# Optimization experiments

Hardware: AMD Instinct MI355X
Metric: run time of the kernel (lower is better)

Reference implementation:

```python
import jax, jax.numpy as jnp
import numpy as np

NUM_HEADS = 8


def setup_inputs() -> dict:
    key = jax.random.key(0)
    k1, k2, k3 = jax.random.split(key, 3)
    B, C, D, H, W = 2, 512, 32, 32, 32
    x = jax.random.normal(k1, (B, C, D, H, W), dtype=jnp.float32)
    w_qkv = jax.random.normal(k2, (3 * C, C), dtype=jnp.float32) * 0.02
    b_qkv = jnp.zeros((3 * C,), dtype=jnp.float32)
    w_out = jax.random.normal(k3, (C, C), dtype=jnp.float32) * 0.02
    b_out = jnp.zeros((C,), dtype=jnp.float32)
    return {"x": x, "w_qkv": w_qkv, "b_qkv": b_qkv, "w_out": w_out, "b_out": b_out}


def reference(x, w_qkv, b_qkv, w_out, b_out):
    B, C, D, H, W = x.shape
    nh = NUM_HEADS
    hd = C // nh
    # 1x1x1 conv3d == pointwise linear over channel dim
    qkv = jnp.einsum('bcdhw,oc->bodhw', x, w_qkv) + b_qkv[None, :, None, None, None]
    q, k, v = jnp.split(qkv, 3, axis=1)  # each [B,C,D,H,W]

    def to_heads(t):
        # [B,C,D,H,W] -> [B,nh,hd,D,H,W] -> [B,H,W,nh,D,hd]
        return t.reshape(B, nh, hd, D, H, W).transpose(0, 4, 5, 1, 3, 2)

    q, k, v = to_heads(q), to_heads(k), to_heads(v)
    scale = hd ** -0.5
    # attention along the depth axis D: attn [B,H,W,nh,D,D]
    attn = jnp.einsum('bhwnic,bhwnjc->bhwnij', q, k) * scale
    attn = jax.nn.softmax(attn, axis=-1)
    out = jnp.einsum('bhwnij,bhwnjc->bhwnic', attn, v)  # [B,H,W,nh,D,hd]
    # [B,H,W,nh,D,hd] -> [B,nh,hd,D,H,W] -> [B,C,D,H,W]
    out = out.transpose(0, 3, 5, 4, 1, 2).reshape(B, C, D, H, W)
    out = jnp.einsum('bcdhw,oc->bodhw', out, w_out) + b_out[None, :, None, None, None]
    return out + x
```

## Files before the change

### kernel.cpp

```cpp
#include <hip/hip_runtime.h>


typedef __bf16 bf16x8 __attribute__((ext_vector_type(8)));
typedef float  f32x4  __attribute__((ext_vector_type(4)));
typedef float  f32x16 __attribute__((ext_vector_type(16)));

__device__ __forceinline__ float b2f(unsigned int u) {
    union { float f; unsigned int i; } x; x.i = u << 16; return x.f;
}
__device__ __forceinline__ unsigned short f2b(float f) {
    union { float f; unsigned int i; } x; x.f = f;
    unsigned int r = x.i + 0x7FFFu + ((x.i >> 16) & 1u);
    return (unsigned short)(r >> 16);
}
__device__ __forceinline__ unsigned int cvtpk(float lo, float hi) {
    unsigned int r;
    asm("v_cvt_pk_bf16_f32 %0, %1, %2" : "=v"(r) : "v"(lo), "v"(hi));
    return r;
}
__device__ __forceinline__ f32x4 mfma16(bf16x8 a, bf16x8 b, f32x4 c) {
    return __builtin_amdgcn_mfma_f32_16x16x32_bf16(a, b, c, 0, 0, 0);
}
__device__ __forceinline__ f32x16 mfma32(bf16x8 a, bf16x8 b, f32x16 c) {
    return __builtin_amdgcn_mfma_f32_32x32x16_bf16(a, b, c, 0, 0, 0);
}
__device__ __forceinline__ void gload16(const void* g, void* l) {
    __builtin_amdgcn_global_load_lds((const unsigned int*)g, (unsigned int*)l, 16, 0, 0);
}

__global__ __launch_bounds__(256) void xprep3(const float* __restrict__ x,
                                              const float* __restrict__ wq_f,
                                              const float* __restrict__ wo_f,
                                              unsigned short* __restrict__ xB,
                                              unsigned short* __restrict__ wT,
                                              unsigned short* __restrict__ wo_bf) {
    const int bid = blockIdx.x;
    const int tid = threadIdx.x;
    if (bid < 2048) {
        __shared__ __align__(16) char tile[32768];
        const int ck = bid & 7, dq = (bid >> 3) & 3, h = (bid >> 5) & 31, b = bid >> 10;

        const int cg = tid & 31;
        const int dl = tid >> 5;
        const int d  = dq * 8 + dl;
        const float* p0 = x + (size_t)b * 16777216 + (size_t)(ck * 64 + cg * 2) * 32768 + d * 1024 + h * 32;
        const float* p1 = p0 + 32768;
        const int cb = (cg * 4) ^ (dl << 4);
        #pragma unroll
        for (int k = 0; k < 8; ++k) {
            float4 a0 = *(const float4*)(p0 + 4 * k);
            float4 a1 = *(const float4*)(p1 + 4 * k);
            *(unsigned int*)(tile + dl * 4096 + (4 * k + 0) * 128 + cb) = cvtpk(a0.x, a1.x);
            *(unsigned int*)(tile + dl * 4096 + (4 * k + 1) * 128 + cb) = cvtpk(a0.y, a1.y);
            *(unsigned int*)(tile + dl * 4096 + (4 * k + 2) * 128 + cb) = cvtpk(a0.z, a1.z);
            *(unsigned int*)(tile + dl * 4096 + (4 * k + 3) * 128 + cb) = cvtpk(a0.w, a1.w);
        }
        __syncthreads();
        const int odl = tid & 7, ot = (tid >> 3) & 7, okb = tid >> 6;
        #pragma unroll
        for (int i = 0; i < 8; ++i) {
            const int wg = i >> 1, kkl = i & 1;
            const int cbyte = (kkl * 64 + okb * 16) ^ (odl << 4);
            uint4 v = *(const uint4*)(tile + odl * 4096 + (wg * 8 + ot) * 128 + cbyte);
            const int G  = (b * 32 + h) * 4 + wg;
            const int kk = ck * 2 + kkl;
            *(uint4*)(xB + (size_t)G * 131072 + kk * 8192 + okb * 2048 +
                      (ot * 32 + dq * 8 + odl) * 8) = v;
        }
    } else {
        const int gidx = (bid - 2048) * 256 + tid;
        if (gidx < 98304) {
            const int r  = gidx % 192;
            const int qd = gidx / 192;
            const int kb = qd & 3, kk = (qd >> 2) & 15, n = qd >> 6;
            const int R  = (r >> 6) * 512 + n * 64 + (r & 63);
            const float* s = wq_f + R * 512 + kk * 32 + kb * 8;
            float4 a0 = *(const float4*)s;
            float4 a1 = *(const float4*)(s + 4);
            *(uint4*)(wT + (size_t)gidx * 8) =
                make_uint4(cvtpk(a0.x, a0.y), cvtpk(a0.z, a0.w), cvtpk(a1.x, a1.y), cvtpk(a1.z, a1.w));
        } else {
            const int g2 = gidx - 98304;
            const float* s = wo_f + (size_t)g2 * 8;
            float4 a0 = *(const float4*)s;
            float4 a1 = *(const float4*)(s + 4);
            *(uint4*)(wo_bf + (size_t)g2 * 8) =
                make_uint4(cvtpk(a0.x, a0.y), cvtpk(a0.z, a0.w), cvtpk(a1.x, a1.y), cvtpk(a1.z, a1.w));
        }
    }
}

__global__ __launch_bounds__(256, 2)
void axial_ab4(const unsigned short* __restrict__ xB,
               const unsigned short* __restrict__ wT,
               const float* __restrict__ bq,
               unsigned short* __restrict__ ao)
{
    __shared__ __align__(16) char lds[74496];
    const int SA0 = 0, SB0 = 24576;
    const int QT0 = 0, KT0 = 16384, VT0 = 32768, P0 = 49152, BIAS0 = 73728;
    float* bias_s = (float*)(lds + BIAS0);

    const int bid = blockIdx.x;
    const int vid = (bid & 7) * 256 + (bid >> 3);
    const int n   = vid & 7;
    const int G   = vid >> 3;
    const int b   = G >> 7, h = (G >> 2) & 31, wg = G & 3;
    const int sbase = b * 32768 + h * 32 + wg * 8;

    const int tid = threadIdx.x;
    const int wv  = tid >> 6;
    const int l   = tid & 63;
    const int l31 = l & 31;
    const int hh  = l >> 5;
    const int wm  = wv >> 1;
    const int wn  = wv & 1;

    const unsigned short* wA = wT + (size_t)n * 98304;
    const unsigned short* xG = xB + (size_t)G * 131072;

    auto stageA = [&](int kk, int sl) {
        #pragma unroll
        for (int i = 0; i < 3; ++i) {
            const int j = wv * 3 + i;
            gload16(wA + kk * 6144 + j * 512 + l * 8, lds + SA0 + sl * 12288 + j * 1024);
        }
    };
    auto stageB = [&](int kk, int sl) {
        #pragma unroll
        for (int i = 0; i < 4; ++i) {
            const int j = wv * 4 + i;
            gload16(xG + kk * 8192 + j * 512 + l * 8, lds + SB0 + sl * 16384 + j * 1024);
        }
    };

    f32x16 acc[3][4];
    #pragma unroll
    for (int mf = 0; mf < 3; ++mf)
        #pragma unroll
        for (int nf = 0; nf < 4; ++nf) acc[mf][nf] = (f32x16)0.f;

    auto gphase = [&](int sa, int sb) {
        #pragma unroll
        for (int ks = 0; ks < 2; ++ks) {
            const int kb = ks * 2 + hh;
            bf16x8 af[3], bfr[4];
            #pragma unroll
            for (int mf = 0; mf < 3; ++mf)
                af[mf] = *(const bf16x8*)(lds + SA0 + sa * 12288 + kb * 3072 +
                                          (wm * 96 + mf * 32 + l31) * 16);
            #pragma unroll
            for (int nf = 0; nf < 4; ++nf)
                bfr[nf] = *(const bf16x8*)(lds + SB0 + sb * 16384 + kb * 4096 +
                                           (wn * 128 + nf * 32 + l31) * 16);
            #pragma unroll
            for (int mf = 0; mf < 3; ++mf)
                #pragma unroll
                for (int nf = 0; nf < 4; ++nf)
                    acc[mf][nf] = mfma32(af[mf], bfr[nf], acc[mf][nf]);
        }
    };

    stageA(0, 0); stageB(0, 0); stageB(1, 1);
    asm volatile("s_waitcnt vmcnt(4)" ::: "memory");
    __builtin_amdgcn_s_barrier();
    __builtin_amdgcn_sched_barrier(0);

    #pragma unroll
    for (int kk = 0; kk < 16; ++kk) {
        if (kk < 15) stageA(kk + 1, (kk + 1) & 1);
        if (kk < 14) stageB(kk + 2, (kk + 2) % 3);
        __builtin_amdgcn_s_setprio(1);
        gphase(kk & 1, kk % 3);
        __builtin_amdgcn_s_setprio(0);
        asm volatile("s_waitcnt lgkmcnt(0)" ::: "memory");
        if (kk < 14)       { asm volatile("s_waitcnt vmcnt(4)" ::: "memory"); }
        else if (kk == 14) { asm volatile("s_waitcnt vmcnt(0)" ::: "memory"); }
        __builtin_amdgcn_s_barrier();
        __builtin_amdgcn_sched_barrier(0);
    }

    if (tid < 192) bias_s[tid] = bq[(tid >> 6) * 512 + n * 64 + (tid & 63)];
    __syncthreads();

    #pragma unroll
    for (int ph = 0; ph < 2; ++ph) {
        if (wn == ph) {
            #pragma unroll
            for (int mf = 0; mf < 3; ++mf) {
                const int m0 = wm * 96 + mf * 32;
                #pragma unroll
                for (int nf = 0; nf < 4; ++nf) {
                    const int tl = nf;
                    const int d  = l31;
                    const f32x16 v = acc[mf][nf];
                    if (m0 < 128) {
                        const int base = (m0 < 64) ? QT0 : KT0;
                        const int c0g  = (m0 & 63) >> 3;
                        #pragma unroll
                        for (int p = 0; p < 4; ++p) {
                            float4 bb = *(const float4*)(bias_s + m0 + 8 * p + 4 * hh);
                            unsigned int u0 = cvtpk(v[4 * p]     + bb.x, v[4 * p + 1] + bb.y);
                            unsigned int u1 = cvtpk(v[4 * p + 2] + bb.z, v[4 * p + 3] + bb.w);
                            *(uint2*)(lds + base + tl * 4096 + d * 128 +
                                      (((c0g + p) ^ (d & 7)) << 4) + 8 * hh) = make_uint2(u0, u1);
                        }
                    } else {
                        const int e0 = m0 - 128;
                        const int jj = tl * 32 + l31;
                        #pragma unroll
                        for (int reg = 0; reg < 16; ++reg) {
                            const int e = e0 + (reg & 3) + 8 * (reg >> 2) + 4 * hh;
                            *(unsigned short*)(lds + VT0 + e * 256 +
                                               (((jj >> 3) ^ (e & 7)) << 4) + ((2 * jj) & 15)) =
                                f2b(v[reg]);
                        }
                    }
                }
            }
        }
        __syncthreads();

        {
            const int t  = wv;
            const int qg = l >> 4;
            f32x4 sacc[2][2];
            sacc[0][0] = (f32x4)0.f; sacc[0][1] = (f32x4)0.f;
            sacc[1][0] = (f32x4)0.f; sacc[1][1] = (f32x4)0.f;
            #pragma unroll
            for (int kh = 0; kh < 2; ++kh) {
                bf16x8 qa[2], kb_[2];
                #pragma unroll
                for (int mt = 0; mt < 2; ++mt) {
                    const int i = mt * 16 + (l & 15);
                    qa[mt] = *(const bf16x8*)(lds + QT0 + t * 4096 + i * 128 +
                                              (((kh * 4 + qg) ^ (i & 7)) << 4));
                }
                #pragma unroll
                for (int nt = 0; nt < 2; ++nt) {
                    const int jj = nt * 16 + (l & 15);
                    kb_[nt] = *(const bf16x8*)(lds + KT0 + t * 4096 + jj * 128 +
                                               (((kh * 4 + qg) ^ (jj & 7)) << 4));
                }
                #pragma unroll
                for (int mt = 0; mt < 2; ++mt)
                    #pragma unroll
                    for (int nt = 0; nt < 2; ++nt)
                        sacc[mt][nt] = mfma16(qa[mt], kb_[nt], sacc[mt][nt]);
            }
            #pragma unroll
            for (int mt = 0; mt < 2; ++mt) {
                #pragma unroll
                for (int reg = 0; reg < 4; ++reg) {
                    float s0 = sacc[mt][0][reg] * 0.125f;
                    float s1 = sacc[mt][1][reg] * 0.125f;
                    float m = fmaxf(s0, s1);
                    m = fmaxf(m, __shfl_xor(m, 1));
                    m = fmaxf(m, __shfl_xor(m, 2));
                    m = fmaxf(m, __shfl_xor(m, 4));
                    m = fmaxf(m, __shfl_xor(m, 8));
                    float p0 = __expf(s0 - m);
                    float p1 = __expf(s1 - m);
                    float ss = p0 + p1;
                    ss += __shfl_xor(ss, 1);
                    ss += __shfl_xor(ss, 2);
                    ss += __shfl_xor(ss, 4);
                    ss += __shfl_xor(ss, 8);
                    float inv = 1.0f / ss;
                    const int i = mt * 16 + 4 * qg + reg;
                    #pragma unroll
                    for (int nt = 0; nt < 2; ++nt) {
                        const int j = nt * 16 + (l & 15);
                        *(unsigned short*)(lds + P0 + t * 2048 + i * 64 +
                                           (((j >> 3) ^ (i & 3)) << 4) + ((2 * j) & 15)) =
                            f2b((nt ? p1 : p0) * inv);
                    }
                }
            }
            asm volatile("s_waitcnt lgkmcnt(0)" ::: "memory");
            __builtin_amdgcn_sched_barrier(0);

            f32x16 oa[2];
            oa[0] = (f32x16)0.f; oa[1] = (f32x16)0.f;
            #pragma unroll
            for (int ks = 0; ks < 2; ++ks) {
                bf16x8 pb = *(const bf16x8*)(lds + P0 + t * 2048 + l31 * 64 +
                                             (((ks * 2 + hh) ^ (l31 & 3)) << 4));
                #pragma unroll
                for (int cf = 0; cf < 2; ++cf) {
                    const int c = cf * 32 + l31;
                    bf16x8 vv = *(const bf16x8*)(lds + VT0 + c * 256 +
                                                 (((t * 4 + ks * 2 + hh) ^ (c & 7)) << 4));
                    oa[cf] = mfma32(vv, pb, oa[cf]);
                }
            }
            const size_t srow = (size_t)(sbase + l31 * 1024 + ph * 4 + t) * 512 + n * 64;
            #pragma unroll
            for (int cf = 0; cf < 2; ++cf) {
                #pragma unroll
                for (int p = 0; p < 4; ++p) {
                    const int cb = cf * 32 + 8 * p + 4 * hh;
                    float4 bb = *(const float4*)(bias_s + 128 + cb);
                    unsigned int u0 = cvtpk(oa[cf][4 * p]     + bb.x, oa[cf][4 * p + 1] + bb.y);
                    unsigned int u1 = cvtpk(oa[cf][4 * p + 2] + bb.z, oa[cf][4 * p + 3] + bb.w);
                    *(uint2*)(ao + srow + cb) = make_uint2(u0, u1);
                }
            }
        }
        __syncthreads();
    }
}

__global__ __launch_bounds__(256, 2)
void axial_out(const unsigned short* __restrict__ ao,
               const unsigned short* __restrict__ wo,
               const float* __restrict__ bo,
               const float* __restrict__ x,
               float* __restrict__ out)
{
    __shared__ __align__(16) char lds[65536];
    const int bid = blockIdx.x;
    const int vid = (bid & 7) * 256 + (bid >> 3);
    const int mt_ = vid & 3;
    const int nt_ = vid >> 2;
    const int m_base = mt_ * 128;
    const int s_base = nt_ * 128;
    const int bb  = s_base >> 15;
    const int spl = s_base & 32767;
    const float* xblk = x + (size_t)bb * 16777216 + spl;
    float* oblk = out + (size_t)bb * 16777216 + spl;

    const int tid = threadIdx.x;
    const int wv  = tid >> 6;
    const int l   = tid & 63;
    const int l31 = l & 31;
    const int hh  = l >> 5;
    const int wm  = wv >> 1;
    const int wn  = wv & 1;

    auto stage = [&](int kk, int buf) {
        #pragma unroll
        for (int i = 0; i < 4; ++i) {
            const int il  = wv * 4 + i;
            const int row = il * 8 + (l >> 3);
            const unsigned short* srcA = wo + (m_base + row) * 512 + kk * 64 +
                                         (((l & 7) ^ (row & 7)) << 3);
            gload16(srcA, lds + buf * 16384 + il * 1024);
            const unsigned short* srcB = ao + (size_t)(s_base + row) * 512 + kk * 64 +
                                         (((l & 7) ^ (row & 7)) << 3);
            gload16(srcB, lds + 32768 + buf * 16384 + il * 1024);
        }
    };

    f32x16 acc[2][2];
    acc[0][0] = (f32x16)0.f; acc[0][1] = (f32x16)0.f;
    acc[1][0] = (f32x16)0.f; acc[1][1] = (f32x16)0.f;

    stage(0, 0);
    __syncthreads();
    int cur = 0;
    for (int kk = 0; kk < 8; ++kk) {
        if (kk < 7) stage(kk + 1, cur ^ 1);
        #pragma unroll
        for (int ks = 0; ks < 4; ++ks) {
            bf16x8 af[2], bfr[2];
            #pragma unroll
            for (int mf = 0; mf < 2; ++mf) {
                const int row = wm * 64 + mf * 32 + l31;
                af[mf] = *(const bf16x8*)(lds + cur * 16384 + row * 128 +
                                          (((ks * 2 + hh) ^ (row & 7)) << 4));
            }
            #pragma unroll
            for (int nf = 0; nf < 2; ++nf) {
                const int row = wn * 64 + nf * 32 + l31;
                bfr[nf] = *(const bf16x8*)(lds + 32768 + cur * 16384 + row * 128 +
                                           (((ks * 2 + hh) ^ (row & 7)) << 4));
            }
            #pragma unroll
            for (int mf = 0; mf < 2; ++mf)
                #pragma unroll
                for (int nf = 0; nf < 2; ++nf)
                    acc[mf][nf] = mfma32(af[mf], bfr[nf], acc[mf][nf]);
        }
        __syncthreads();
        cur ^= 1;
    }

    #pragma unroll
    for (int mf = 0; mf < 2; ++mf) {
        #pragma unroll
        for (int reg = 0; reg < 16; ++reg) {
            const int co = m_base + wm * 64 + mf * 32 + (reg & 3) + 8 * (reg >> 2) + 4 * hh;
            const float bias = bo[co];
            #pragma unroll
            for (int nf = 0; nf < 2; ++nf) {
                const int sl = wn * 64 + nf * 32 + l31;
                oblk[(size_t)co * 32768 + sl] = acc[mf][nf][reg] + bias +
                                                xblk[(size_t)co * 32768 + sl];
            }
        }
    }
}

__global__ __launch_bounds__(256) void wconvert(const float* __restrict__ wq,
                                                const float* __restrict__ wo,
                                                unsigned short* __restrict__ dst) {
    int i = blockIdx.x * 256 + threadIdx.x;
    const float* src;
    int off;
    if (i < 196608) { src = wq; off = i * 4; }
    else            { src = wo; off = (i - 196608) * 4; }
    float4 v = *(const float4*)(src + off);
    *(uint2*)(dst + (size_t)i * 4) = make_uint2(cvtpk(v.x, v.y), cvtpk(v.z, v.w));
}

__device__ __forceinline__ int adr_qk(int row, int cb) { return row * 2048 + (cb ^ ((row & 7) << 4)); }
__device__ __forceinline__ int adr_x (int row, int cb) { return 98304 + row * 1024 + (cb ^ ((row & 7) << 4)); }
__device__ __forceinline__ int adr_xl(int row, int cb) { return 131072 + row * 1024 + (cb ^ ((row & 7) << 4)); }
__device__ __forceinline__ int adr_v (int e, int jb)   { int a = e * 64 + jb; return 65536 + (a ^ ((e & 7) << 4)); }

__global__ __launch_bounds__(512, 1)
void axial3d_mfma(const float* __restrict__ x,
                  const float* __restrict__ bq,
                  const float* __restrict__ bo,
                  const unsigned short* __restrict__ wq,
                  const unsigned short* __restrict__ wo,
                  float* __restrict__ out) {
    __shared__ char lds[163840];
    const int bid  = blockIdx.x;
    const int work = (bid & 7) * 256 + (bid >> 3);
    const int b    = work >> 10;
    const int h    = (work >> 5) & 31;
    const int w    = work & 31;
    const float* xb = x   + ((size_t)b * 16777216u) + h * 32 + w;
    float*       ob = out + ((size_t)b * 16777216u) + h * 32 + w;
    const int tid  = threadIdx.x;
    const int wv   = tid >> 6;
    const int lane = tid & 63;
    const int g    = lane >> 4;
    const int q    = lane & 15;
    {
        const int d  = tid & 31;
        const int c0 = tid >> 5;
        #pragma unroll
        for (int it = 0; it < 32; ++it) {
            int c = c0 + it * 16;
            float xv = xb[c * 32768 + d * 1024];
            unsigned short hi = f2b(xv);
            unsigned short lo = f2b(xv - b2f(hi));
            *(unsigned short*)(lds + adr_x(d, c * 2))  = hi;
            *(unsigned short*)(lds + adr_xl(d, c * 2)) = lo;
        }
    }
    __syncthreads();
    for (int tp = 0; tp < 3; ++tp) {
        const int mt0 = wv * 12 + tp * 4;
        f32x4 acc[4][2];
        #pragma unroll
        for (int t = 0; t < 4; ++t) { acc[t][0] = (f32x4)0.f; acc[t][1] = (f32x4)0.f; }
        #pragma unroll
        for (int kk = 0; kk < 16; ++kk) {
            bf16x8 bfr[2];
            #pragma unroll
            for (int nt = 0; nt < 2; ++nt)
                bfr[nt] = *(const bf16x8*)(lds + adr_x(nt * 16 + q, kk * 64 + g * 16));
            #pragma unroll
            for (int t = 0; t < 4; ++t) {
                const int o = (mt0 + t) * 16 + q;
                bf16x8 a = *(const bf16x8*)((const char*)wq + o * 1024 + kk * 64 + g * 16);
                acc[t][0] = mfma16(a, bfr[0], acc[t][0]);
                acc[t][1] = mfma16(a, bfr[1], acc[t][1]);
            }
        }
        #pragma unroll
        for (int t = 0; t < 4; ++t) {
            const int mt    = mt0 + t;
            const int obase = mt * 16 + 4 * g;
            float bias[4];
            #pragma unroll
            for (int r = 0; r < 4; ++r) bias[r] = bq[obase + r];
            if (mt < 64) {
                #pragma unroll
                for (int nt = 0; nt < 2; ++nt) {
                    const int d = nt * 16 + q;
                    unsigned int lo = f2b(acc[t][nt][0] + bias[0]) |
                                      ((unsigned int)f2b(acc[t][nt][1] + bias[1]) << 16);
                    unsigned int hi = f2b(acc[t][nt][2] + bias[2]) |
                                      ((unsigned int)f2b(acc[t][nt][3] + bias[3]) << 16);
                    *(uint2*)(lds + adr_qk(d, obase * 2)) = make_uint2(lo, hi);
                }
            } else {
                #pragma unroll
                for (int nt = 0; nt < 2; ++nt) {
                    const int d = nt * 16 + q;
                    #pragma unroll
                    for (int r = 0; r < 4; ++r) {
                        const int e = obase + r - 1024;
                        *(unsigned short*)(lds + adr_v(e, d * 2)) = f2b(acc[t][nt][r] + bias[r]);
                    }
                }
            }
        }
    }
    __syncthreads();
    {
        const int n = wv;
        f32x4 s[2][2];
        s[0][0] = (f32x4)0.f; s[0][1] = (f32x4)0.f;
        s[1][0] = (f32x4)0.f; s[1][1] = (f32x4)0.f;
        #pragma unroll
        for (int kk = 0; kk < 2; ++kk) {
            bf16x8 a0 = *(const bf16x8*)(lds + adr_qk(q,      n * 128 + kk * 64 + g * 16));
            bf16x8 a1 = *(const bf16x8*)(lds + adr_qk(16 + q, n * 128 + kk * 64 + g * 16));
            bf16x8 b0 = *(const bf16x8*)(lds + adr_qk(q,      1024 + n * 128 + kk * 64 + g * 16));
            bf16x8 b1 = *(const bf16x8*)(lds + adr_qk(16 + q, 1024 + n * 128 + kk * 64 + g * 16));
            s[0][0] = mfma16(a0, b0, s[0][0]);
            s[0][1] = mfma16(a0, b1, s[0][1]);
            s[1][0] = mfma16(a1, b0, s[1][0]);
            s[1][1] = mfma16(a1, b1, s[1][1]);
        }
        float pv[2][2][4];
        #pragma unroll
        for (int it = 0; it < 2; ++it) {
            #pragma unroll
            for (int r = 0; r < 4; ++r) {
                float s0 = s[it][0][r] * 0.125f;
                float s1 = s[it][1][r] * 0.125f;
                float m = fmaxf(s0, s1);
                m = fmaxf(m, __shfl_xor(m, 1));
                m = fmaxf(m, __shfl_xor(m, 2));
                m = fmaxf(m, __shfl_xor(m, 4));
                m = fmaxf(m, __shfl_xor(m, 8));
                float p0 = __expf(s0 - m);
                float p1 = __expf(s1 - m);
                float ss = p0 + p1;
                ss += __shfl_xor(ss, 1);
                ss += __shfl_xor(ss, 2);
                ss += __shfl_xor(ss, 4);
                ss += __shfl_xor(ss, 8);
                float inv = 1.0f / ss;
                pv[it][0][r] = p0 * inv;
                pv[it][1][r] = p1 * inv;
            }
        }
        #pragma unroll
        for (int it = 0; it < 2; ++it)
            #pragma unroll
            for (int jt = 0; jt < 2; ++jt)
                #pragma unroll
                for (int r = 0; r < 4; ++r) {
                    const int i = it * 16 + 4 * g + r;
                    *(unsigned short*)(lds + adr_qk(i, n * 128 + (jt * 16 + q) * 2)) =
                        f2b(pv[it][jt][r]);
                }
        asm volatile("s_waitcnt lgkmcnt(0)" ::: "memory");
        __builtin_amdgcn_sched_barrier(0);
        bf16x8 pa0 = *(const bf16x8*)(lds + adr_qk(q,      n * 128 + g * 16));
        bf16x8 pa1 = *(const bf16x8*)(lds + adr_qk(16 + q, n * 128 + g * 16));
        #pragma unroll
        for (int et = 0; et < 4; ++et) {
            const int e = n * 64 + et * 16 + q;
            bf16x8 vb = *(const bf16x8*)(lds + adr_v(e, g * 16));
            f32x4 o0 = mfma16(pa0, vb, (f32x4)0.f);
            f32x4 o1 = mfma16(pa1, vb, (f32x4)0.f);
            const int cb = 1024 + n * 128 + (et * 16 + q) * 2;
            #pragma unroll
            for (int r = 0; r < 4; ++r) {
                *(unsigned short*)(lds + adr_qk(4 * g + r, cb))      = f2b(o0[r]);
                *(unsigned short*)(lds + adr_qk(16 + 4 * g + r, cb)) = f2b(o1[r]);
            }
        }
    }
    __syncthreads();
    for (int p4 = 0; p4 < 4; ++p4) {
        const int mt = wv * 4 + p4;
        f32x4 acc[2];
        acc[0] = (f32x4)0.f; acc[1] = (f32x4)0.f;
        #pragma unroll
        for (int kk = 0; kk < 16; ++kk) {
            bf16x8 b0 = *(const bf16x8*)(lds + adr_qk(q,      1024 + kk * 64 + g * 16));
            bf16x8 b1 = *(const bf16x8*)(lds + adr_qk(16 + q, 1024 + kk * 64 + g * 16));
            bf16x8 a  = *(const bf16x8*)((const char*)wo + (mt * 16 + q) * 1024 + kk * 64 + g * 16);
            acc[0] = mfma16(a, b0, acc[0]);
            acc[1] = mfma16(a, b1, acc[1]);
        }
        const int obase = mt * 16 + 4 * g;
        float bias[4];
        #pragma unroll
        for (int r = 0; r < 4; ++r) bias[r] = bo[obase + r];
        #pragma unroll
        for (int nt = 0; nt < 2; ++nt) {
            const int d = nt * 16 + q;
            uint2 xh = *(const uint2*)(lds + adr_x(d, obase * 2));
            uint2 xl = *(const uint2*)(lds + adr_xl(d, obase * 2));
            float res[4];
            res[0] = b2f(xh.x & 0xffffu) + b2f(xl.x & 0xffffu);
            res[1] = b2f(xh.x >> 16)     + b2f(xl.x >> 16);
            res[2] = b2f(xh.y & 0xffffu) + b2f(xl.y & 0xffffu);
            res[3] = b2f(xh.y >> 16)     + b2f(xl.y >> 16);
            #pragma unroll
            for (int r = 0; r < 4; ++r)
                ob[(obase + r) * 32768 + d * 1024] = acc[nt][r] + bias[r] + res[r];
        }
    }
}

extern "C" void kernel_launch(void* const* d_in, const int* in_sizes, int n_in,
                              void* d_out, int out_size, void* d_ws, size_t ws_size,
                              hipStream_t stream) {
    const float* x     = (const float*)d_in[0];
    const float* w_qkv = (const float*)d_in[1];
    const float* b_qkv = (const float*)d_in[2];
    const float* w_out = (const float*)d_in[3];
    const float* b_out = (const float*)d_in[4];
    float* out = (float*)d_out;

    const size_t XB_OFF = 0;
    const size_t AO_OFF = 67108864;
    const size_t WT_OFF = 134217728;
    const size_t NEED   = 136314880;

    if (ws_size >= NEED) {
        unsigned short* xB    = (unsigned short*)((char*)d_ws + XB_OFF);
        unsigned short* ao    = (unsigned short*)((char*)d_ws + AO_OFF);
        unsigned short* wTt   = (unsigned short*)((char*)d_ws + WT_OFF);
        unsigned short* wo_bf = wTt + 786432;
        xprep3   <<<dim3(2560), dim3(256), 0, stream>>>(x, w_qkv, w_out, xB, wTt, wo_bf);
        axial_ab4<<<dim3(2048), dim3(256), 0, stream>>>(xB, wTt, b_qkv, ao);
        axial_out<<<dim3(2048), dim3(256), 0, stream>>>(ao, wo_bf, b_out, x, out);
    } else {
        unsigned short* wbf = (unsigned short*)d_ws;
        wconvert<<<dim3(1024), dim3(256), 0, stream>>>(w_qkv, w_out, wbf);
        axial3d_mfma<<<dim3(2048), dim3(512), 0, stream>>>(x, b_qkv, b_out,
                                                           wbf, wbf + 786432, out);
    }
}
```

Measured before the change: 273.2 us.

## Restructure QKV GEMM main loop into interleaved LDS-read and MFMA clusters with barriers

```diff
diff --git a/kernel.cpp b/kernel.cpp
--- a/kernel.cpp
+++ b/kernel.cpp
@@ -91,7 +91,7 @@
 }
 
 __global__ __launch_bounds__(256, 2)
-void axial_ab4(const unsigned short* __restrict__ xB,
+void axial_ab5(const unsigned short* __restrict__ xB,
                const unsigned short* __restrict__ wT,
                const float* __restrict__ bq,
                unsigned short* __restrict__ ao)
@@ -140,44 +140,56 @@
         #pragma unroll
         for (int nf = 0; nf < 4; ++nf) acc[mf][nf] = (f32x16)0.f;
 
-    auto gphase = [&](int sa, int sb) {
-        #pragma unroll
-        for (int ks = 0; ks < 2; ++ks) {
-            const int kb = ks * 2 + hh;
-            bf16x8 af[3], bfr[4];
-            #pragma unroll
-            for (int mf = 0; mf < 3; ++mf)
-                af[mf] = *(const bf16x8*)(lds + SA0 + sa * 12288 + kb * 3072 +
-                                          (wm * 96 + mf * 32 + l31) * 16);
+    auto dsread = [&](int sa, int sb, int ks, bf16x8* af, bf16x8* bfr) {
+        const int kb = ks * 2 + hh;
+        #pragma unroll
+        for (int mf = 0; mf < 3; ++mf)
+            af[mf] = *(const bf16x8*)(lds + SA0 + sa * 12288 + kb * 3072 +
+                                      (wm * 96 + mf * 32 + l31) * 16);
+        #pragma unroll
+        for (int nf = 0; nf < 4; ++nf)
+            bfr[nf] = *(const bf16x8*)(lds + SB0 + sb * 16384 + kb * 4096 +
+                                       (wn * 128 + nf * 32 + l31) * 16);
+    };
+    auto mcluster = [&](bf16x8* af, bf16x8* bfr) {
+        __builtin_amdgcn_s_setprio(1);
+        #pragma unroll
+        for (int mf = 0; mf < 3; ++mf)
             #pragma unroll
             for (int nf = 0; nf < 4; ++nf)
-                bfr[nf] = *(const bf16x8*)(lds + SB0 + sb * 16384 + kb * 4096 +
-                                           (wn * 128 + nf * 32 + l31) * 16);
-            #pragma unroll
-            for (int mf = 0; mf < 3; ++mf)
-                #pragma unroll
-                for (int nf = 0; nf < 4; ++nf)
-                    acc[mf][nf] = mfma32(af[mf], bfr[nf], acc[mf][nf]);
-        }
+                acc[mf][nf] = mfma32(af[mf], bfr[nf], acc[mf][nf]);
+        __builtin_amdgcn_s_setprio(0);
     };
 
-    stageA(0, 0); stageB(0, 0); stageB(1, 1);
-    asm volatile("s_waitcnt vmcnt(4)" ::: "memory");
+    stageA(0, 0); stageB(0, 0);
+    stageA(1, 1); stageB(1, 1);
+    asm volatile("s_waitcnt vmcnt(7)" ::: "memory");
     __builtin_amdgcn_s_barrier();
     __builtin_amdgcn_sched_barrier(0);
 
     #pragma unroll
     for (int kk = 0; kk < 16; ++kk) {
+        const int sa = kk & 1, sb = kk % 3;
+        bf16x8 af[3], bfr[4];
+        dsread(sa, sb, 0, af, bfr);
         if (kk < 15) stageA(kk + 1, (kk + 1) & 1);
-        if (kk < 14) stageB(kk + 2, (kk + 2) % 3);
-        __builtin_amdgcn_s_setprio(1);
-        gphase(kk & 1, kk % 3);
-        __builtin_amdgcn_s_setprio(0);
+        __builtin_amdgcn_s_barrier();
         asm volatile("s_waitcnt lgkmcnt(0)" ::: "memory");
-        if (kk < 14)       { asm volatile("s_waitcnt vmcnt(4)" ::: "memory"); }
-        else if (kk == 14) { asm volatile("s_waitcnt vmcnt(0)" ::: "memory"); }
+        __builtin_amdgcn_sched_barrier(0);
+        mcluster(af, bfr);
         __builtin_amdgcn_s_barrier();
+        dsread(sa, sb, 1, af, bfr);
+        if (kk < 14) {
+            stageB(kk + 2, (kk + 2) % 3);
+            asm volatile("s_waitcnt vmcnt(4)" ::: "memory");
+        } else if (kk == 14) {
+            asm volatile("s_waitcnt vmcnt(0)" ::: "memory");
+        }
+        __builtin_amdgcn_s_barrier();
+        asm volatile("s_waitcnt lgkmcnt(0)" ::: "memory");
         __builtin_amdgcn_sched_barrier(0);
+        mcluster(af, bfr);
+        __builtin_amdgcn_s_barrier();
     }
 
     if (tid < 192) bias_s[tid] = bq[(tid >> 6) * 512 + n * 64 + (tid & 63)];
@@ -474,7 +486,7 @@
         }
         #pragma unroll
         for (int t = 0; t < 4; ++t) {
-            const int mt    = mt0 + t;
+            const int mt    = tp * 4 + t + wv * 12;
             const int obase = mt * 16 + 4 * g;
             float bias[4];
             #pragma unroll
@@ -626,7 +638,7 @@
         unsigned short* wTt   = (unsigned short*)((char*)d_ws + WT_OFF);
         unsigned short* wo_bf = wTt + 786432;
         xprep3   <<<dim3(2560), dim3(256), 0, stream>>>(x, w_qkv, w_out, xB, wTt, wo_bf);
-        axial_ab4<<<dim3(2048), dim3(256), 0, stream>>>(xB, wTt, b_qkv, ao);
+        axial_ab5<<<dim3(2048), dim3(256), 0, stream>>>(xB, wTt, b_qkv, ao);
         axial_out<<<dim3(2048), dim3(256), 0, stream>>>(ao, wo_bf, b_out, x, out);
     } else {
         unsigned short* wbf = (unsigned short*)d_ws;
```

New measurement: 285.4 us. +4.5%, slower.
